# Kernel optimization log

Measured on AMD Instinct MI355X. Metric: run time of the kernel, lower is better.

Reference implementation:

```python
import jax, jax.numpy as jnp
import numpy as np

B, L2, CONV, D, SD, RES, MAXD = 2, 1024, 4, 256, 3, 32, 6
L1, L0 = 8 * L2, 64 * L2
S = L2 + L1 + L0


def setup_inputs():
    key = jax.random.key(0)
    ks = jax.random.split(key, 10)
    # fully 'mixed' octree: every token value is 2 (no padding), which satisfies the
    # substitution count constraints len1 = 8*len2, len0 = 8*len1 exactly.
    value = jnp.full((B, S), 2, dtype=jnp.int32)
    depth = jnp.concatenate([
        jnp.full((B, L2), MAXD - 2, jnp.int32),
        jnp.full((B, L1), MAXD - 1, jnp.int32),
        jnp.full((B, L0), MAXD, jnp.int32)], axis=1)
    position = jax.random.randint(ks[0], (B, S, SD), 1, RES + 1, dtype=jnp.int32)

    def emb(k, n):
        t = 0.02 * jax.random.normal(k, (n, D), jnp.float32)
        return t.at[0].set(0.0)  # padding row '0'

    emb_val = emb(ks[1], 4)            # num_vocab=3 (+ padding token 0)
    emb_dep = emb(ks[2], MAXD + 2)
    emb_pos = jnp.stack([emb(ks[3 + i], RES + 1) for i in range(SD)])  # (SD, RES+1, D)

    def conv_w(k, s):
        return jax.random.normal(k, (D, D, s), jnp.float32) / np.sqrt(D * s)

    W0, b0 = conv_w(ks[6], 8), jnp.zeros((D,), jnp.float32)
    W1, b1 = conv_w(ks[7], 8), jnp.zeros((D,), jnp.float32)
    W2, b2 = conv_w(ks[8], CONV), jnp.zeros((D,), jnp.float32)
    return dict(value=value, depth=depth, position=position,
                emb_val=emb_val, emb_dep=emb_dep, emb_pos=emb_pos,
                W0=W0, b0=b0, W1=W1, b1=b1, W2=W2, b2=b2,
                len2=L2, len1=L1, len0=L0, conv_size=CONV)


def _conv(x, W, b, s):
    # Conv1d(D, D, kernel=s, stride=s) over channel-last layout
    Bb, L, Dd = x.shape
    xr = x.reshape(Bb, L // s, s, Dd)
    return jnp.einsum('blkd,odk->blo', xr, W) + b


def _substitute(x_tgt, val_tgt, y_src, val_src_head):
    # x_tgt[val_tgt==2] = y_src[val_src_head != 0]  (per batch row, in order)
    mask_sub = val_tgt == 2                                     # (B, Lt)
    mask_src = val_src_head != 0                                # (B, Ls)
    order = jnp.argsort(jnp.where(mask_src, 0, 1), axis=1)      # stable: valid rows first
    y_c = jnp.take_along_axis(y_src, order[:, :, None], axis=1)
    idx = jnp.clip(jnp.cumsum(mask_sub.astype(jnp.int32), axis=1) - 1, 0, y_src.shape[1] - 1)
    sub = jnp.take_along_axis(y_c, idx[:, :, None], axis=1)
    return jnp.where(mask_sub[:, :, None], sub, x_tgt)


def _forward(value, depth, position, emb_val, emb_dep, emb_pos,
             W0, b0, W1, b1, W2, b2, len2, len1, len0, conv_size):
    e = emb_val[value] + emb_dep[depth]
    for i in range(SD):
        e = e + emb_pos[i][position[..., i]]
    # static split into three depth levels (equal lengths per batch row)
    x2, x1, x0 = e[:, :len2], e[:, len2:len2 + len1], e[:, len2 + len1:]
    v2, v1, v0 = value[:, :len2], value[:, len2:len2 + len1], value[:, len2 + len1:]

    y0 = _conv(x0, W0, b0, 8)                  # (B, len0//8, D)
    x1 = _substitute(x1, v1, y0, v0[:, ::8])
    y1 = _conv(x1, W1, b1, 8)                  # (B, len1//8, D)
    x2 = _substitute(x2, v2, y1, v1[:, ::8])
    x_out = _conv(x2, W2, b2, conv_size)       # (B, len2//c, D)

    # mask of output groups that contain a mixed token with existing children
    Bb = value.shape[0]
    m1 = jnp.any(v1.reshape(Bb, -1, 8) == 2, axis=-1)           # (B, len1//8)
    is2 = v2 == 2
    idx = jnp.clip(jnp.cumsum(is2.astype(jnp.int32), axis=1) - 1, 0, m1.shape[1] - 1)
    m2 = jnp.where(is2, jnp.take_along_axis(m1, idx, axis=1), False)
    m2g = jnp.any(m2.reshape(Bb, -1, conv_size), axis=-1)       # (B, len2//c)

    Lout = len2 // conv_size  # == max(sum(m2g)) for fully-mixed octrees
    order = jnp.argsort(jnp.where(m2g, 0, 1), axis=1)
    xg = jnp.take_along_axis(x_out, order[:, :, None], axis=1)[:, :Lout]
    valid = jnp.arange(Lout)[None, :] < jnp.sum(m2g, axis=1, keepdims=True)
    return jnp.where(valid[:, :, None], xg, 0.0)


def reference(value, depth, position, emb_val, emb_dep, emb_pos,
              W0, b0, W1, b1, W2, b2, len2, len1, len0, conv_size):
    return _forward(value, depth, position, emb_val, emb_dep, emb_pos,
                    W0, b0, W1, b1, W2, b2, len2, len1, len0, conv_size)
```

## Files before the change

kernel.cpp:

```cpp
#include <hip/hip_runtime.h>
#include <stdint.h>


#define SEQT 74752

typedef __attribute__((ext_vector_type(8))) short bf16x8;
typedef __attribute__((ext_vector_type(4))) float f32x4;

__device__ __forceinline__ unsigned short f2bf(float f) {
  union { float f; unsigned u; } v; v.f = f;
  unsigned r = v.u + 0x7FFFu + ((v.u >> 16) & 1u);
  return (unsigned short)(r >> 16);
}

__device__ __forceinline__ void gload_lds16(const unsigned short* g, unsigned short* l) {
  __builtin_amdgcn_global_load_lds(
      (const __attribute__((address_space(1))) void*)g,
      (__attribute__((address_space(3))) void*)l, 16, 0, 0);
}

__device__ __forceinline__ void mfma_quad(const unsigned short* sAc, const unsigned short* sBc,
    int wm, int wn, int quad, int l16, f32x4 acc[2][2]) {
#pragma unroll
  for (int ks = 0; ks < 2; ++ks) {
    bf16x8 a0, a1, b0f, b1f; int row;
    row = wm * 32 + l16;      a0  = *(const bf16x8*)&sAc[row * 64 + (((ks * 4 + quad) ^ (row & 7)) * 8)];
    row = wm * 32 + 16 + l16; a1  = *(const bf16x8*)&sAc[row * 64 + (((ks * 4 + quad) ^ (row & 7)) * 8)];
    row = wn * 32 + l16;      b0f = *(const bf16x8*)&sBc[row * 64 + (((ks * 4 + quad) ^ (row & 7)) * 8)];
    row = wn * 32 + 16 + l16; b1f = *(const bf16x8*)&sBc[row * 64 + (((ks * 4 + quad) ^ (row & 7)) * 8)];
    acc[0][0] = __builtin_amdgcn_mfma_f32_16x16x32_bf16(a0, b0f, acc[0][0], 0, 0, 0);
    acc[0][1] = __builtin_amdgcn_mfma_f32_16x16x32_bf16(a0, b1f, acc[0][1], 0, 0, 0);
    acc[1][0] = __builtin_amdgcn_mfma_f32_16x16x32_bf16(a1, b0f, acc[1][0], 0, 0, 0);
    acc[1][1] = __builtin_amdgcn_mfma_f32_16x16x32_bf16(a1, b1f, acc[1][1], 0, 0, 0);
  }
}

__device__ __forceinline__ void build_sB(unsigned short* sBf, const float* W,
    int rowOrigin, int rowStride, int colStride, int colOfs, int t) {
  const int r = t >> 2, q = t & 3;
  const float* rp = W + (long)(rowOrigin + r) * rowStride + colOfs;
#pragma unroll
  for (int kc = 0; kc < 4; ++kc)
#pragma unroll
    for (int gg = 0; gg < 2; ++gg) {
      const int g = q * 2 + gg;
      const int c0 = kc * 64 + g * 8;
      unsigned short tmp[8];
#pragma unroll
      for (int e = 0; e < 8; ++e) tmp[e] = f2bf(rp[(long)(c0 + e) * colStride]);
      *(uint4*)&sBf[kc * 4096 + r * 64 + ((g ^ (r & 7)) * 8)] = *(uint4*)tmp;
    }
}

__device__ __forceinline__ void build_sB2(unsigned short* sBf, const float* W,
    int rowOrigin, int rowStride, int colStride, int colOfs, int t, int kcBase) {
  const int r = t >> 2, q = t & 3;
  const float* rp = W + (long)(rowOrigin + r) * rowStride + colOfs;
#pragma unroll
  for (int kl = 0; kl < 2; ++kl) {
    const int kc = kcBase + kl;
#pragma unroll
    for (int gg = 0; gg < 2; ++gg) {
      const int g = q * 2 + gg;
      const int c0 = kc * 64 + g * 8;
      unsigned short tmp[8];
#pragma unroll
      for (int e = 0; e < 8; ++e) tmp[e] = f2bf(rp[(long)(c0 + e) * colStride]);
      *(uint4*)&sBf[kl * 4096 + r * 64 + ((g ^ (r & 7)) * 8)] = *(uint4*)tmp;
    }
  }
}

__global__ __launch_bounds__(256) void u0self_k(
    const float* __restrict__ ev, const float* __restrict__ ed,
    const float* __restrict__ ep, const float* __restrict__ W0,
    const float* __restrict__ b0, const float* __restrict__ b1,
    unsigned short* __restrict__ U, float* __restrict__ C1,
    int* __restrict__ sem) {
  __shared__ __attribute__((aligned(16))) unsigned short sBf[2 * 4096];
  __shared__ __attribute__((aligned(16))) unsigned short sAf[2 * 4096];
  const int bid = blockIdx.x, t = threadIdx.x;
  if (bid == 64) { C1[t] = b1[t]; if (t < 32) sem[t] = 0; return; }
  const int wave = t >> 6, lane = t & 63;
  const int wm = wave >> 1, wn = wave & 1;
  const int quad = lane >> 4, l16 = lane & 15;
  const int bm = bid & 1, bn = bid >> 1;

  f32x4 acc[2][2] = {};
#pragma unroll
  for (int half = 0; half < 2; ++half) {
    {
      const int r = t >> 2, q = t & 3;
      const int ip = bm * 64 + r;
      const float* rowp = (ip < 4)   ? ev + (long)ip * 256
                        : (ip < 12)  ? ed + (long)(ip - 4) * 256
                        : (ip < 111) ? ep + (long)(ip - 12) * 256
                                     : (const float*)0;
#pragma unroll
      for (int kl = 0; kl < 2; ++kl) {
        const int kc = half * 2 + kl;
#pragma unroll
        for (int gg = 0; gg < 2; ++gg) {
          const int g = q * 2 + gg, c0 = kc * 64 + g * 8;
          unsigned short tmp[8];
#pragma unroll
          for (int e = 0; e < 8; ++e) tmp[e] = rowp ? f2bf(rowp[c0 + e]) : (unsigned short)0;
          *(uint4*)&sAf[kl * 4096 + r * 64 + ((g ^ (r & 7)) * 8)] = *(uint4*)tmp;
        }
      }
    }
    build_sB2(sBf, W0, (bn & 3) * 64, 2048, 8, bn >> 2, t, half * 2);
    __syncthreads();
    mfma_quad(sAf,        sBf,        wm, wn, quad, l16, acc);
    mfma_quad(sAf + 4096, sBf + 4096, wm, wn, quad, l16, acc);
    __syncthreads();
  }

  for (int i = 0; i < 2; ++i)
    for (int j = 0; j < 2; ++j) {
      int col = bn * 64 + wn * 32 + j * 16 + l16;
      for (int r = 0; r < 4; ++r) {
        int row = bm * 64 + wm * 32 + i * 16 + quad * 4 + r;
        if (row < 111) U[(long)row * 2048 + col] = f2bf(acc[i][j][r]);
        else if (row == 111)
          U[(long)row * 2048 + col] = (col < 256) ? f2bf(b0[col]) : (unsigned short)0;
      }
    }
}

__global__ __launch_bounds__(256) void vgemm_self_k(
    const unsigned short* __restrict__ A, const float* __restrict__ W1,
    unsigned short* __restrict__ V, float* __restrict__ C1) {
  __shared__ __attribute__((aligned(16))) unsigned short sBf[4 * 4096];
  __shared__ __attribute__((aligned(16))) unsigned short sA[2 * 4096];
  __shared__ float sC1[64];
  const int bm = blockIdx.x, bn = blockIdx.y;
  const int t = threadIdx.x;
  const int wave = t >> 6, lane = t & 63;
  const int wm = wave >> 1, wn = wave & 1;
  const int quad = lane >> 4, l16 = lane & 15;
  const int srow = t >> 3, scol = ((t & 7) ^ (srow & 7)) * 8;
  const int lofs = t * 8;

  build_sB(sBf, W1, (bn & 3) * 64, 2048, 8, bn >> 2, t);
  if (t < 64) sC1[t] = 0.0f;
  const unsigned short* Ab = A + (long)(bm * 64 + srow) * 256 + scol;
  f32x4 acc[2][2] = {};
  auto issueA = [&](int it, int buf) {
    const long ko = (long)it * 64;
    gload_lds16(Ab + ko,                  sA + buf * 4096 + lofs);
    gload_lds16(Ab + ko + (long)32 * 256, sA + buf * 4096 + lofs + 2048);
  };
  issueA(0, 0);
  for (int it = 0; it < 4; ++it) {
    const int cur = it & 1;
    __syncthreads();
    if (it + 1 < 4) issueA(it + 1, cur ^ 1);
    mfma_quad(sA + cur * 4096, sBf + it * 4096, wm, wn, quad, l16, acc);
  }
  const bool hasC1 = (bm == 0) || (bm == 1) || (bm == 13);
  for (int i = 0; i < 2; ++i)
    for (int j = 0; j < 2; ++j) {
      int lc = wn * 32 + j * 16 + l16;
      int col = bn * 64 + lc;
      for (int r = 0; r < 4; ++r) {
        int row = bm * 64 + wm * 32 + i * 16 + quad * 4 + r;
        float val = acc[i][j][r];
        V[(long)row * 2048 + col] = f2bf(val);
        if (hasC1) {
          bool cst = (row == 888) || (row >= 16 && row < 24) || (row >= 80 && row < 88);
          if (cst) atomicAdd(&sC1[lc], val);
        }
      }
    }
  if (hasC1) {
    __syncthreads();
    if (t < 64) atomicAdd(&C1[(bn * 64 + t) & 255], sC1[t]);
  }
}

__device__ __forceinline__ void addslice(float acc[8], const unsigned short* p) {
  const uint4 u = *(const uint4*)p;
  union { unsigned u; float f; } c;
  c.u = u.x << 16;          acc[0] += c.f;
  c.u = u.x & 0xFFFF0000u;  acc[1] += c.f;
  c.u = u.y << 16;          acc[2] += c.f;
  c.u = u.y & 0xFFFF0000u;  acc[3] += c.f;
  c.u = u.z << 16;          acc[4] += c.f;
  c.u = u.z & 0xFFFF0000u;  acc[5] += c.f;
  c.u = u.w << 16;          acc[6] += c.f;
  c.u = u.w & 0xFFFF0000u;  acc[7] += c.f;
}

__global__ __launch_bounds__(256) void gather1_k(
    const int* __restrict__ position,
    const unsigned short* __restrict__ V, const float* __restrict__ C1,
    unsigned short* __restrict__ y1) {
  __shared__ int sidx[192];
  __shared__ float sacc[8 * 256];
  const int t = threadIdx.x;
  const int row = blockIdx.x;
  const int b = row >> 10, rr = row & 1023;
  const long qb3 = ((long)b * SEQT + 9216 + (long)rr * 64) * 3;
  if (t < 192) sidx[t] = position[qb3 + t];
  __syncthreads();

  const int wg = t >> 5, cg = t & 31, o0 = cg * 8;
  float acc[8] = {};
  const int* si = &sidx[wg * 24];
  const unsigned short* Vbase = V + wg * 256 + o0;
#pragma unroll
  for (int k = 0; k < 8; ++k) {
    const int p0 = si[k * 3], p1 = si[k * 3 + 1], p2 = si[k * 3 + 2];
    const unsigned short* Vw = Vbase + k * 2048;
    addslice(acc, Vw + (12 + p0) * 16384);
    addslice(acc, Vw + (45 + p1) * 16384);
    addslice(acc, Vw + (78 + p2) * 16384);
  }
  *(float4*)&sacc[wg * 256 + o0]     = make_float4(acc[0], acc[1], acc[2], acc[3]);
  *(float4*)&sacc[wg * 256 + o0 + 4] = make_float4(acc[4], acc[5], acc[6], acc[7]);
  __syncthreads();

  float s = C1[t];
#pragma unroll
  for (int w = 0; w < 8; ++w) s += sacc[w * 256 + t];
  y1[(long)row * 256 + t] = f2bf(s);
}

__global__ __launch_bounds__(256) void gemm64f_self_k(
    const unsigned short* __restrict__ A, const float* __restrict__ W2,
    float* __restrict__ C, const float* __restrict__ b2,
    float* __restrict__ out, int* __restrict__ sem) {
  const int N = 256;
  const long MN = (long)512 * N;
  __shared__ __attribute__((aligned(16))) unsigned short sBf[4 * 4096];
  __shared__ __attribute__((aligned(16))) unsigned short sA[2 * 4096];
  const int bm = blockIdx.x, bn = blockIdx.y, z = blockIdx.z;
  const int t = threadIdx.x;
  const int wave = t >> 6, lane = t & 63;
  const int wm = wave >> 1, wn = wave & 1;
  const int quad = lane >> 4, l16 = lane & 15;
  const int srow = t >> 3, scol = ((t & 7) ^ (srow & 7)) * 8;
  const int lofs = t * 8;

  float* Cz = C + (long)z * MN;
  build_sB(sBf, W2, bn * 64, 1024, 4, z, t);
  const unsigned short* Ab = A + (long)(bm * 64 + srow) * 1024 + z * 256 + scol;
  f32x4 acc[2][2] = {};
  auto issueA = [&](int it, int buf) {
    const long ko = (long)it * 64;
    gload_lds16(Ab + ko,                   sA + buf * 4096 + lofs);
    gload_lds16(Ab + ko + (long)32 * 1024, sA + buf * 4096 + lofs + 2048);
  };
  issueA(0, 0);
  for (int it = 0; it < 4; ++it) {
    const int cur = it & 1;
    __syncthreads();
    if (it + 1 < 4) issueA(it + 1, cur ^ 1);
    mfma_quad(sA + cur * 4096, sBf + it * 4096, wm, wn, quad, l16, acc);
  }
  for (int i = 0; i < 2; ++i)
    for (int j = 0; j < 2; ++j) {
      int col = bn * 64 + wn * 32 + j * 16 + l16;
      for (int r = 0; r < 4; ++r) {
        int row = bm * 64 + wm * 32 + i * 16 + quad * 4 + r;
        Cz[(long)row * N + col] = acc[i][j][r];
      }
    }

  __threadfence();
  __shared__ int sold;
  if (t == 0) sold = atomicAdd(&sem[bm * 4 + bn], 1);
  __syncthreads();
  if (sold == 3) {
    __threadfence();
    for (int idx = t; idx < 4096; idx += 256) {
      int r = idx >> 6, c = idx & 63;
      int row = bm * 64 + r, col = bn * 64 + c;
      float s = b2[col];
#pragma unroll
      for (int zz = 0; zz < 4; ++zz) s += C[zz * MN + (long)row * N + col];
      out[(long)row * N + col] = s;
    }
  }
}

extern "C" void kernel_launch(void* const* d_in, const int* in_sizes, int n_in,
                              void* d_out, int out_size, void* d_ws, size_t ws_size,
                              hipStream_t stream) {
  const int*   position = (const int*)d_in[2];
  const float* emb_val  = (const float*)d_in[3];
  const float* emb_dep  = (const float*)d_in[4];
  const float* emb_pos  = (const float*)d_in[5];
  const float* W0 = (const float*)d_in[6];
  const float* b0 = (const float*)d_in[7];
  const float* W1 = (const float*)d_in[8];
  const float* b1 = (const float*)d_in[9];
  const float* W2 = (const float*)d_in[10];
  const float* b2 = (const float*)d_in[11];
  float* out = (float*)d_out;

  unsigned short* U  = (unsigned short*)d_ws;
  unsigned short* V  = U + 229376;
  unsigned short* y1 = V + 1835008;
  float* C1  = (float*)(y1 + 524288);
  float* y2p = C1 + 512;
  int*   sem = (int*)(y2p + 4L * 131072);

  u0self_k<<<65, 256, 0, stream>>>(emb_val, emb_dep, emb_pos, W0, b0, b1, U, C1, sem);
  vgemm_self_k<<<dim3(14, 32), 256, 0, stream>>>(U, W1, V, C1);
  gather1_k<<<2048, 256, 0, stream>>>(position, V, C1, y1);
  gemm64f_self_k<<<dim3(8, 4, 4), 256, 0, stream>>>(y1, W2, y2p, b2, out, sem);
}
```

Measured before the change: 161.9 us.

## Pre-transpose W1/W2 to bf16 in prep kernel and stream B tiles via LDS DMA

Adds extra blocks to the first kernel that convert W1 and W2 to bf16 in a K-contiguous transposed layout in workspace. The two GEMM kernels then load B tiles with double-buffered global-to-LDS loads instead of each block doing strided fp32 gathers and conversions of the weights. This removes redundant per-block weight conversion and uncoalesced strided reads, at the cost of an extra workspace write/read of the converted weights and more blocks in the first kernel.

Measured after the change: 143.3 us. 11.5% less time.

```diff
diff --git a/kernel.cpp b/kernel.cpp
--- a/kernel.cpp
+++ b/kernel.cpp
@@ -35,12 +35,13 @@
   }
 }
 
-__device__ __forceinline__ void build_sB(unsigned short* sBf, const float* W,
-    int rowOrigin, int rowStride, int colStride, int colOfs, int t) {
+__device__ __forceinline__ void build_sB2(unsigned short* sBf, const float* W,
+    int rowOrigin, int rowStride, int colStride, int colOfs, int t, int kcBase) {
   const int r = t >> 2, q = t & 3;
   const float* rp = W + (long)(rowOrigin + r) * rowStride + colOfs;
 #pragma unroll
-  for (int kc = 0; kc < 4; ++kc)
+  for (int kl = 0; kl < 2; ++kl) {
+    const int kc = kcBase + kl;
 #pragma unroll
     for (int gg = 0; gg < 2; ++gg) {
       const int g = q * 2 + gg;
@@ -48,39 +49,45 @@
       unsigned short tmp[8];
 #pragma unroll
       for (int e = 0; e < 8; ++e) tmp[e] = f2bf(rp[(long)(c0 + e) * colStride]);
-      *(uint4*)&sBf[kc * 4096 + r * 64 + ((g ^ (r & 7)) * 8)] = *(uint4*)tmp;
-    }
-}
-
-__device__ __forceinline__ void build_sB2(unsigned short* sBf, const float* W,
-    int rowOrigin, int rowStride, int colStride, int colOfs, int t, int kcBase) {
-  const int r = t >> 2, q = t & 3;
-  const float* rp = W + (long)(rowOrigin + r) * rowStride + colOfs;
-#pragma unroll
-  for (int kl = 0; kl < 2; ++kl) {
-    const int kc = kcBase + kl;
-#pragma unroll
-    for (int gg = 0; gg < 2; ++gg) {
-      const int g = q * 2 + gg;
-      const int c0 = kc * 64 + g * 8;
-      unsigned short tmp[8];
-#pragma unroll
-      for (int e = 0; e < 8; ++e) tmp[e] = f2bf(rp[(long)(c0 + e) * colStride]);
       *(uint4*)&sBf[kl * 4096 + r * 64 + ((g ^ (r & 7)) * 8)] = *(uint4*)tmp;
     }
   }
 }
 
-__global__ __launch_bounds__(256) void u0self_k(
+__global__ __launch_bounds__(256) void u0prep_k(
     const float* __restrict__ ev, const float* __restrict__ ed,
     const float* __restrict__ ep, const float* __restrict__ W0,
     const float* __restrict__ b0, const float* __restrict__ b1,
-    unsigned short* __restrict__ U, float* __restrict__ C1,
+    const float* __restrict__ W1, const float* __restrict__ W2,
+    unsigned short* __restrict__ U, unsigned short* __restrict__ w1v,
+    unsigned short* __restrict__ wt2, float* __restrict__ C1,
     int* __restrict__ sem) {
   __shared__ __attribute__((aligned(16))) unsigned short sBf[2 * 4096];
   __shared__ __attribute__((aligned(16))) unsigned short sAf[2 * 4096];
   const int bid = blockIdx.x, t = threadIdx.x;
+
   if (bid == 64) { C1[t] = b1[t]; if (t < 32) sem[t] = 0; return; }
+  if (bid >= 321) {
+    const int o = bid - 321;
+#pragma unroll
+    for (int i = 0; i < 4; ++i) sBf[i * 256 + t] = f2bf(W2[o * 1024 + i * 256 + t]);
+    __syncthreads();
+#pragma unroll
+    for (int k = 0; k < 4; ++k)
+      wt2[o * 1024 + (k << 8) + t] = sBf[t * 4 + k];
+    return;
+  }
+  if (bid >= 65) {
+    const int o = bid - 65;
+#pragma unroll
+    for (int i = 0; i < 8; ++i) sBf[i * 256 + t] = f2bf(W1[o * 2048 + i * 256 + t]);
+    __syncthreads();
+#pragma unroll
+    for (int j2 = 0; j2 < 8; ++j2)
+      w1v[(j2 * 256 + o) * 256 + t] = sBf[t * 8 + j2];
+    return;
+  }
+
   const int wave = t >> 6, lane = t & 63;
   const int wm = wave >> 1, wn = wave & 1;
   const int quad = lane >> 4, l16 = lane & 15;
@@ -128,36 +135,47 @@
     }
 }
 
-__global__ __launch_bounds__(256) void vgemm_self_k(
-    const unsigned short* __restrict__ A, const float* __restrict__ W1,
-    unsigned short* __restrict__ V, float* __restrict__ C1) {
-  __shared__ __attribute__((aligned(16))) unsigned short sBf[4 * 4096];
-  __shared__ __attribute__((aligned(16))) unsigned short sA[2 * 4096];
+__global__ __launch_bounds__(256) void vgemm_k(
+    const unsigned short* __restrict__ A, const unsigned short* __restrict__ Bt,
+    unsigned short* __restrict__ C, float* __restrict__ C1) {
+  const int K = 256, N = 2048;
+  __shared__ __attribute__((aligned(16))) unsigned short sA[2][64 * 64];
+  __shared__ __attribute__((aligned(16))) unsigned short sB[2][64 * 64];
   __shared__ float sC1[64];
   const int bm = blockIdx.x, bn = blockIdx.y;
+
   const int t = threadIdx.x;
   const int wave = t >> 6, lane = t & 63;
   const int wm = wave >> 1, wn = wave & 1;
   const int quad = lane >> 4, l16 = lane & 15;
-  const int srow = t >> 3, scol = ((t & 7) ^ (srow & 7)) * 8;
+
+  const int srow = t >> 3;
+  const int scol = (((t & 7) ^ (srow & 7)) * 8);
   const int lofs = t * 8;
 
-  build_sB(sBf, W1, (bn & 3) * 64, 2048, 8, bn >> 2, t);
   if (t < 64) sC1[t] = 0.0f;
-  const unsigned short* Ab = A + (long)(bm * 64 + srow) * 256 + scol;
+
+  const unsigned short* Ab = A + (long)(bm * 64 + srow) * K + scol;
+  const unsigned short* Bb = Bt + (long)(bn * 64 + srow) * K + scol;
+
   f32x4 acc[2][2] = {};
-  auto issueA = [&](int it, int buf) {
+
+  auto issue_tile = [&](int it, int buf) {
     const long ko = (long)it * 64;
-    gload_lds16(Ab + ko,                  sA + buf * 4096 + lofs);
-    gload_lds16(Ab + ko + (long)32 * 256, sA + buf * 4096 + lofs + 2048);
+    gload_lds16(Ab + ko,                sA[buf] + lofs);
+    gload_lds16(Ab + ko + (long)32 * K, sA[buf] + lofs + 2048);
+    gload_lds16(Bb + ko,                sB[buf] + lofs);
+    gload_lds16(Bb + ko + (long)32 * K, sB[buf] + lofs + 2048);
   };
-  issueA(0, 0);
+
+  issue_tile(0, 0);
   for (int it = 0; it < 4; ++it) {
     const int cur = it & 1;
     __syncthreads();
-    if (it + 1 < 4) issueA(it + 1, cur ^ 1);
-    mfma_quad(sA + cur * 4096, sBf + it * 4096, wm, wn, quad, l16, acc);
-  }
+    if (it + 1 < 4) issue_tile(it + 1, cur ^ 1);
+    mfma_quad(sA[cur], sB[cur], wm, wn, quad, l16, acc);
+  }
+
   const bool hasC1 = (bm == 0) || (bm == 1) || (bm == 13);
   for (int i = 0; i < 2; ++i)
     for (int j = 0; j < 2; ++j) {
@@ -166,7 +184,7 @@
       for (int r = 0; r < 4; ++r) {
         int row = bm * 64 + wm * 32 + i * 16 + quad * 4 + r;
         float val = acc[i][j][r];
-        V[(long)row * 2048 + col] = f2bf(val);
+        C[(long)row * N + col] = f2bf(val);
         if (hasC1) {
           bool cst = (row == 888) || (row >= 16 && row < 24) || (row >= 80 && row < 88);
           if (cst) atomicAdd(&sC1[lc], val);
@@ -227,38 +245,48 @@
   y1[(long)row * 256 + t] = f2bf(s);
 }
 
-__global__ __launch_bounds__(256) void gemm64f_self_k(
-    const unsigned short* __restrict__ A, const float* __restrict__ W2,
+__global__ __launch_bounds__(256) void gemm64f_k(
+    const unsigned short* __restrict__ A, const unsigned short* __restrict__ Bt,
     float* __restrict__ C, const float* __restrict__ b2,
     float* __restrict__ out, int* __restrict__ sem) {
-  const int N = 256;
+  const int N = 256, K = 1024, kLen = 256;
   const long MN = (long)512 * N;
-  __shared__ __attribute__((aligned(16))) unsigned short sBf[4 * 4096];
-  __shared__ __attribute__((aligned(16))) unsigned short sA[2 * 4096];
-  const int bm = blockIdx.x, bn = blockIdx.y, z = blockIdx.z;
+  __shared__ __attribute__((aligned(16))) unsigned short sA[2][64 * 64];
+  __shared__ __attribute__((aligned(16))) unsigned short sB[2][64 * 64];
+  const int bm = blockIdx.x, bn = blockIdx.y;
+  const int kBase = blockIdx.z * kLen;
+  float* Cz = C + (long)blockIdx.z * MN;
+
   const int t = threadIdx.x;
   const int wave = t >> 6, lane = t & 63;
   const int wm = wave >> 1, wn = wave & 1;
   const int quad = lane >> 4, l16 = lane & 15;
-  const int srow = t >> 3, scol = ((t & 7) ^ (srow & 7)) * 8;
+
+  const int srow = t >> 3;
+  const int scol = (((t & 7) ^ (srow & 7)) * 8);
   const int lofs = t * 8;
 
-  float* Cz = C + (long)z * MN;
-  build_sB(sBf, W2, bn * 64, 1024, 4, z, t);
-  const unsigned short* Ab = A + (long)(bm * 64 + srow) * 1024 + z * 256 + scol;
+  const unsigned short* Ab = A + (long)(bm * 64 + srow) * K + kBase + scol;
+  const unsigned short* Bb = Bt + (long)(bn * 64 + srow) * K + kBase + scol;
+
   f32x4 acc[2][2] = {};
-  auto issueA = [&](int it, int buf) {
+
+  auto issue_tile = [&](int it, int buf) {
     const long ko = (long)it * 64;
-    gload_lds16(Ab + ko,                   sA + buf * 4096 + lofs);
-    gload_lds16(Ab + ko + (long)32 * 1024, sA + buf * 4096 + lofs + 2048);
+    gload_lds16(Ab + ko,                sA[buf] + lofs);
+    gload_lds16(Ab + ko + (long)32 * K, sA[buf] + lofs + 2048);
+    gload_lds16(Bb + ko,                sB[buf] + lofs);
+    gload_lds16(Bb + ko + (long)32 * K, sB[buf] + lofs + 2048);
   };
-  issueA(0, 0);
+
+  issue_tile(0, 0);
   for (int it = 0; it < 4; ++it) {
     const int cur = it & 1;
     __syncthreads();
-    if (it + 1 < 4) issueA(it + 1, cur ^ 1);
-    mfma_quad(sA + cur * 4096, sBf + it * 4096, wm, wn, quad, l16, acc);
-  }
+    if (it + 1 < 4) issue_tile(it + 1, cur ^ 1);
+    mfma_quad(sA[cur], sB[cur], wm, wn, quad, l16, acc);
+  }
+
   for (int i = 0; i < 2; ++i)
     for (int j = 0; j < 2; ++j) {
       int col = bn * 64 + wn * 32 + j * 16 + l16;
@@ -279,7 +307,7 @@
       int row = bm * 64 + r, col = bn * 64 + c;
       float s = b2[col];
 #pragma unroll
-      for (int zz = 0; zz < 4; ++zz) s += C[zz * MN + (long)row * N + col];
+      for (int z = 0; z < 4; ++z) s += C[z * MN + (long)row * N + col];
       out[(long)row * N + col] = s;
     }
   }
@@ -300,15 +328,18 @@
   const float* b2 = (const float*)d_in[11];
   float* out = (float*)d_out;
 
-  unsigned short* U  = (unsigned short*)d_ws;
-  unsigned short* V  = U + 229376;
-  unsigned short* y1 = V + 1835008;
-  float* C1  = (float*)(y1 + 524288);
+  unsigned short* U   = (unsigned short*)d_ws;
+  unsigned short* V   = U + 229376;
+  unsigned short* y1  = V + 1835008;
+  unsigned short* w1v = y1 + 524288;
+  unsigned short* wt2 = w1v + 524288;
+  float* C1  = (float*)(wt2 + 262144);
   float* y2p = C1 + 512;
   int*   sem = (int*)(y2p + 4L * 131072);
 
-  u0self_k<<<65, 256, 0, stream>>>(emb_val, emb_dep, emb_pos, W0, b0, b1, U, C1, sem);
-  vgemm_self_k<<<dim3(14, 32), 256, 0, stream>>>(U, W1, V, C1);
+  u0prep_k<<<577, 256, 0, stream>>>(emb_val, emb_dep, emb_pos, W0, b0, b1,
+                                    W1, W2, U, w1v, wt2, C1, sem);
+  vgemm_k<<<dim3(14, 32), 256, 0, stream>>>(U, w1v, V, C1);
   gather1_k<<<2048, 256, 0, stream>>>(position, V, C1, y1);
-  gemm64f_self_k<<<dim3(8, 4, 4), 256, 0, stream>>>(y1, W2, y2p, b2, out, sem);
-}
+  gemm64f_k<<<dim3(8, 4, 4), 256, 0, stream>>>(y1, wt2, y2p, b2, out, sem);
+}
```
